# Kernel optimization log

Measured on AMD Instinct MI355X. Metric: run time of the kernel, lower is better.

The kernel has to match this reference:

```python
import jax, jax.numpy as jnp
import numpy as np

EPS_PRE = 1e-05   # constant added to raw scores in the torch module
EPS_NORM = 1e-12  # F.normalize default eps


def setup_inputs() -> dict:
    key = jax.random.key(0)
    kq, kk, kv = jax.random.split(key, 3)
    B, H, S, D = 2, 8, 2048, 64
    query = jax.random.normal(kq, (B, H, S, D), dtype=jnp.float32)
    keys = jax.random.normal(kk, (B, H, S, D), dtype=jnp.float32)
    vals = jax.random.normal(kv, (B, H, S, D), dtype=jnp.float32)
    # causal mask, broadcastable over batch and heads; mask==0 -> score zeroed
    mask = jnp.tril(jnp.ones((S, S), dtype=jnp.int32))[None, None, :, :]
    return {"query": query, "keys": keys, "vals": vals, "mask": mask}


def reference(query, keys, vals, mask):
    # preattn: [B,H,S,S]
    preattn = jnp.einsum("bhsd,bhtd->bhst", query, keys) + EPS_PRE
    preattn = jnp.where(mask == 0, 0.0, preattn)
    # F.normalize(dim=-1): x / max(||x||_2, eps)
    norm = jnp.sqrt(jnp.sum(preattn * preattn, axis=-1, keepdims=True))
    attn = preattn / jnp.maximum(norm, EPS_NORM)
    # dropout is identity in eval mode (reference baseline)
    out = jnp.einsum("bhst,bhtd->bhsd", attn, vals)
    return (out, attn)
```

## Files before the change

### kernel.cpp

```cpp
#include <hip/hip_runtime.h>

#define S_DIM 2048
#define D_DIM 64
#define BH    16
#define EPS_PRE  1e-5f
#define EPS_NORM 1e-12f
#define CT 8

typedef __attribute__((ext_vector_type(8))) short bf8;
typedef __attribute__((ext_vector_type(4))) float f32x4;

static __device__ __forceinline__ unsigned fbits(float x){ union{float f;unsigned u;}v; v.f=x; return v.u; }
static __device__ __forceinline__ float bcast(unsigned u){ union{unsigned u;float f;}v; v.u=u; return v.f; }

static __device__ __forceinline__ void split2(float x, unsigned short& h, unsigned short& l){
  unsigned u = fbits(x);
  h = (unsigned short)(u >> 16);
  float lo = x - bcast(u & 0xffff0000u);
  l = (unsigned short)(fbits(lo) >> 16);
}

static __device__ __forceinline__ void pack4f(float x0, float x1, float x2, float x3,
                                              uint2& hh, uint2& ll){
  unsigned u0=fbits(x0),u1=fbits(x1),u2=fbits(x2),u3=fbits(x3);
  hh.x = (u0>>16) | (u1 & 0xffff0000u);
  hh.y = (u2>>16) | (u3 & 0xffff0000u);
  float l0 = x0 - bcast(u0&0xffff0000u);
  float l1 = x1 - bcast(u1&0xffff0000u);
  float l2 = x2 - bcast(u2&0xffff0000u);
  float l3 = x3 - bcast(u3&0xffff0000u);
  ll.x = (fbits(l0)>>16) | (fbits(l1)&0xffff0000u);
  ll.y = (fbits(l2)>>16) | (fbits(l3)&0xffff0000u);
}

static __device__ __forceinline__ f32x4 mfma16(bf8 a, bf8 b, f32x4 c){
  return __builtin_amdgcn_mfma_f32_16x16x32_bf16(a, b, c, 0, 0, 0);
}

static __device__ __forceinline__ void decode(int c, int& rb, int& ck, int& nk){
  int g = 0;
  while (c >= 4*(g+1)*(g+2)) ++g;
  const int off = c - 4*g*(g+1);
  nk = g + 1;
  const int q = off / nk;
  rb = g*8 + q;
  ck = off - q*nk;
}

__global__ __launch_bounds__(256, 4)
void lka_norm(const float* __restrict__ Qg, const float* __restrict__ Kg,
              float* __restrict__ ssqg, float* __restrict__ Ag)
{
  __shared__ short kThi[4096], kTlo[4096];

  const int tid = threadIdx.x;
  const int wv  = tid >> 6;
  const int ln  = tid & 63;
  const int gq  = ln >> 4;
  const int i16 = ln & 15;

  const int blk = blockIdx.x;
  const int bh  = blk & 15;
  int rb, ck, nk; decode(blk >> 4, rb, ck, nk);
  const int s0 = rb * 64;

  const float* Qb = Qg + (size_t)bh * (S_DIM * D_DIM);
  const float* Kb = Kg + (size_t)bh * (S_DIM * D_DIM);
  float* Ab = Ag + (size_t)bh * ((size_t)S_DIM * S_DIM);

  const int srow = s0 + wv * 16 + i16;

  {
    const int zt0 = (rb + 1) + ((31 - rb) * ck) / nk;
    const int zt1 = (rb + 1) + ((31 - rb) * (ck + 1)) / nk;
    if (zt1 > zt0) {
      const int r = tid >> 2;
      float4* rowp = (float4*)(Ab + (size_t)(s0 + r) * S_DIM + zt0 * 64);
      const int n4 = (zt1 - zt0) * 16;
      float4 z = make_float4(0.f, 0.f, 0.f, 0.f);
      for (int c4 = tid & 3; c4 < n4; c4 += 4) rowp[c4] = z;
    }
  }

  bf8 qhi[2], qlo[2];
  #pragma unroll
  for (int ks = 0; ks < 2; ++ks) {
    const float* qp = Qb + (size_t)srow * D_DIM + ks * 32 + gq * 8;
    float4 a = *(const float4*)qp;
    float4 b = *(const float4*)(qp + 4);
    union { bf8 v; unsigned short h[8]; } H, L;
    float f0[8] = {a.x,a.y,a.z,a.w,b.x,b.y,b.z,b.w};
    #pragma unroll
    for (int j = 0; j < 8; ++j) split2(f0[j], H.h[j], L.h[j]);
    qhi[ks] = H.v; qlo[ks] = L.v;
  }

  auto stageK = [&](int t0){
    const int t  = tid >> 2;
    const int db = (tid & 3) * 16;
    const float* kp = Kb + (size_t)(t0 + t) * D_DIM + db;
    #pragma unroll
    for (int c = 0; c < 4; ++c) {
      float4 kv = *(const float4*)(kp + 4*c);
      uint2 hh, ll; pack4f(kv.x, kv.y, kv.z, kv.w, hh, ll);
      const int idx = t*64 + ((db + 4*c) ^ ((t & 7) << 3));
      *(uint2*)&kThi[idx] = hh;
      *(uint2*)&kTlo[idx] = ll;
    }
  };

  auto qkstep = [&](f32x4* acc){
    #pragma unroll
    for (int rf = 0; rf < 4; ++rf) acc[rf] = (f32x4){0.f,0.f,0.f,0.f};
    #pragma unroll
    for (int ks = 0; ks < 2; ++ks) {
      #pragma unroll
      for (int rf = 0; rf < 4; ++rf) {
        const int t   = rf*16 + i16;
        const int idx = t*64 + ((ks*32 + gq*8) ^ ((t & 7) << 3));
        bf8 ahi = *(const bf8*)&kThi[idx];
        bf8 alo = *(const bf8*)&kTlo[idx];
        acc[rf] = mfma16(ahi, qhi[ks], acc[rf]);
        acc[rf] = mfma16(alo, qhi[ks], acc[rf]);
        acc[rf] = mfma16(ahi, qlo[ks], acc[rf]);
      }
    }
  };

  float ssq = 0.f;
  const int j0 = ck * CT;
  const int j1 = min(j0 + CT, rb + 1);
  for (int j = j0; j < j1; ++j) {
    __syncthreads();
    stageK(j * 64);
    __syncthreads();
    f32x4 acc[4];
    qkstep(acc);
    if (j == rb) {
      #pragma unroll
      for (int rf = 0; rf < 4; ++rf)
        #pragma unroll
        for (int rg = 0; rg < 4; ++rg) {
          const int t = j*64 + rf*16 + gq*4 + rg;
          const float x = (t <= srow) ? (acc[rf][rg] + EPS_PRE) : 0.f;
          ssq += x * x;
        }
    } else {
      #pragma unroll
      for (int rf = 0; rf < 4; ++rf)
        #pragma unroll
        for (int rg = 0; rg < 4; ++rg) {
          const float x = acc[rf][rg] + EPS_PRE;
          ssq += x * x;
        }
    }
  }
  ssq += __shfl_xor(ssq, 16);
  ssq += __shfl_xor(ssq, 32);
  if (gq == 0)
    atomicAdd(&ssqg[bh * S_DIM + srow], ssq);
}

__global__ __launch_bounds__(256, 3)
void lka_emit(const float* __restrict__ Qg, const float* __restrict__ Kg,
              const float* __restrict__ Vg, const float* __restrict__ ssqg,
              float* __restrict__ Og, float* __restrict__ Ag)
{
  __shared__ short kThi[4096], kTlo[4096];
  __shared__ short vThi[4096], vTlo[4096];
  __shared__ short pHi [4096], pLo [4096];

  const int tid = threadIdx.x;
  const int wv  = tid >> 6;
  const int ln  = tid & 63;
  const int gq  = ln >> 4;
  const int i16 = ln & 15;

  const int blk = blockIdx.x;
  const int bh  = blk & 15;
  int rb, ck, nk; decode(blk >> 4, rb, ck, nk);
  (void)nk;
  const int s0 = rb * 64;

  const float* Qb = Qg + (size_t)bh * (S_DIM * D_DIM);
  const float* Kb = Kg + (size_t)bh * (S_DIM * D_DIM);
  const float* Vb = Vg + (size_t)bh * (S_DIM * D_DIM);
  float* Ob = Og + (size_t)bh * (S_DIM * D_DIM);
  float* Ab = Ag + (size_t)bh * ((size_t)S_DIM * S_DIM);

  const int srow = s0 + wv * 16 + i16;

  const float rinv = 1.f / fmaxf(sqrtf(ssqg[bh * S_DIM + srow]), EPS_NORM);

  bf8 qhi[2], qlo[2];
  #pragma unroll
  for (int ks = 0; ks < 2; ++ks) {
    const float* qp = Qb + (size_t)srow * D_DIM + ks * 32 + gq * 8;
    float4 a = *(const float4*)qp;
    float4 b = *(const float4*)(qp + 4);
    union { bf8 v; unsigned short h[8]; } H, L;
    float f0[8] = {a.x,a.y,a.z,a.w,b.x,b.y,b.z,b.w};
    #pragma unroll
    for (int j = 0; j < 8; ++j) split2(f0[j], H.h[j], L.h[j]);
    qhi[ks] = H.v; qlo[ks] = L.v;
  }

  auto stageK = [&](int t0){
    const int t  = tid >> 2;
    const int db = (tid & 3) * 16;
    const float* kp = Kb + (size_t)(t0 + t) * D_DIM + db;
    #pragma unroll
    for (int c = 0; c < 4; ++c) {
      float4 kv = *(const float4*)(kp + 4*c);
      uint2 hh, ll; pack4f(kv.x, kv.y, kv.z, kv.w, hh, ll);
      const int idx = t*64 + ((db + 4*c) ^ ((t & 7) << 3));
      *(uint2*)&kThi[idx] = hh;
      *(uint2*)&kTlo[idx] = ll;
    }
  };
  auto stageV = [&](int t0){
    const int d  = (tid & 31) * 2;
    const int tb = (tid >> 5) * 8;
    float2 rr[8];
    #pragma unroll
    for (int k = 0; k < 8; ++k)
      rr[k] = *(const float2*)(Vb + (size_t)(t0 + tb + k) * D_DIM + d);
    #pragma unroll
    for (int dd = 0; dd < 2; ++dd) {
      union { bf8 v; unsigned short h[8]; } H, L;
      #pragma unroll
      for (int k = 0; k < 8; ++k) split2(dd ? rr[k].y : rr[k].x, H.h[k], L.h[k]);
      const int dc = d + dd;
      const int idx = dc*64 + (tb ^ ((dc & 7) << 3));
      *(bf8*)&vThi[idx] = H.v;
      *(bf8*)&vTlo[idx] = L.v;
    }
  };

  auto qkstep = [&](f32x4* acc){
    #pragma unroll
    for (int rf = 0; rf < 4; ++rf) acc[rf] = (f32x4){0.f,0.f,0.f,0.f};
    #pragma unroll
    for (int ks = 0; ks < 2; ++ks) {
      #pragma unroll
      for (int rf = 0; rf < 4; ++rf) {
        const int t   = rf*16 + i16;
        const int idx = t*64 + ((ks*32 + gq*8) ^ ((t & 7) << 3));
        bf8 ahi = *(const bf8*)&kThi[idx];
        bf8 alo = *(const bf8*)&kTlo[idx];
        acc[rf] = mfma16(ahi, qhi[ks], acc[rf]);
        acc[rf] = mfma16(alo, qhi[ks], acc[rf]);
        acc[rf] = mfma16(ahi, qlo[ks], acc[rf]);
      }
    }
  };

  f32x4 oacc[4];
  #pragma unroll
  for (int rf = 0; rf < 4; ++rf) oacc[rf] = (f32x4){0.f,0.f,0.f,0.f};

  const int pR = wv*16 + i16;

  const int j0 = ck * CT;
  const int j1 = min(j0 + CT, rb + 1);
  for (int j = j0; j < j1; ++j) {
    __syncthreads();
    stageK(j * 64);
    stageV(j * 64);
    __syncthreads();

    f32x4 acc[4];
    qkstep(acc);

    #pragma unroll
    for (int rf = 0; rf < 4; ++rf) {
      f32x4 x;
      #pragma unroll
      for (int rg = 0; rg < 4; ++rg) {
        const int t = j*64 + rf*16 + gq*4 + rg;
        float v = acc[rf][rg] + EPS_PRE;
        if (j == rb && t > srow) v = 0.f;
        x[rg] = v * rinv;
      }
      *(f32x4*)(Ab + (size_t)srow * S_DIM + j*64 + rf*16 + gq*4) = x;
      uint2 hh, ll; pack4f(x[0], x[1], x[2], x[3], hh, ll);
      const int pidx = pR*64 + ((rf*16 + gq*4) ^ ((pR & 7) << 3));
      *(uint2*)&pHi[pidx] = hh;
      *(uint2*)&pLo[pidx] = ll;
    }

    #pragma unroll
    for (int ks = 0; ks < 2; ++ks) {
      const int pi = pR*64 + ((ks*32 + gq*8) ^ ((pR & 7) << 3));
      bf8 bhi = *(const bf8*)&pHi[pi];
      bf8 blo = *(const bf8*)&pLo[pi];
      #pragma unroll
      for (int rfd = 0; rfd < 4; ++rfd) {
        const int dct = rfd*16 + i16;
        const int vi  = dct*64 + ((ks*32 + gq*8) ^ ((dct & 7) << 3));
        bf8 ahi = *(const bf8*)&vThi[vi];
        bf8 alo = *(const bf8*)&vTlo[vi];
        oacc[rfd] = mfma16(ahi, bhi, oacc[rfd]);
        oacc[rfd] = mfma16(alo, bhi, oacc[rfd]);
        oacc[rfd] = mfma16(ahi, blo, oacc[rfd]);
      }
    }
  }

  #pragma unroll
  for (int rfd = 0; rfd < 4; ++rfd)
    #pragma unroll
    for (int rg = 0; rg < 4; ++rg)
      atomicAdd(&Ob[(size_t)srow * D_DIM + rfd*16 + gq*4 + rg], oacc[rfd][rg]);
}

extern "C" void kernel_launch(void* const* d_in, const int* in_sizes, int n_in,
                              void* d_out, int out_size, void* d_ws, size_t ws_size,
                              hipStream_t stream) {
  (void)in_sizes; (void)n_in; (void)out_size; (void)ws_size;
  const float* Q = (const float*)d_in[0];
  const float* K = (const float*)d_in[1];
  const float* V = (const float*)d_in[2];
  float* out  = (float*)d_out;
  float* attn = out + (size_t)BH * S_DIM * D_DIM;
  float* ssq  = (float*)d_ws;

  hipMemsetAsync(ssq, 0, (size_t)BH * S_DIM * sizeof(float), stream);
  hipMemsetAsync(out, 0, (size_t)BH * S_DIM * D_DIM * sizeof(float), stream);

  const int nblk = BH * 80;
  lka_norm<<<dim3(nblk), dim3(256), 0, stream>>>(Q, K, ssq, attn);
  lka_emit<<<dim3(nblk), dim3(256), 0, stream>>>(Q, K, V, ssq, out, attn);
}
```

Baseline: 388.4 us.

## Compute row norms via prefix Gram matrices of K instead of full QK pass

Replaces the row-norm pass, which recomputed every causal QK^T tile, with an algebraic form. Per-tile Gram matrices K^T K and K column sums are built, prefix-summed across tiles, and combined with a single diagonal-tile QK product. Each row's squared norm then comes from q^T M q plus the eps correction terms. This cuts the norm-pass work from quadratic to linear in sequence length and removes the memsets and atomics, at the cost of three extra launches, a larger workspace, and possible cancellation error from the split-bf16 Gram matrix.

```diff
diff --git a/kernel.cpp b/kernel.cpp
--- a/kernel.cpp
+++ b/kernel.cpp
@@ -6,6 +6,12 @@
 #define EPS_PRE  1e-5f
 #define EPS_NORM 1e-12f
 #define CT 8
+
+#define WS_G   0
+#define WS_M   (BH*32*4096)
+#define WS_GV  (2*BH*32*4096)
+#define WS_MV  (WS_GV + BH*32*64)
+#define WS_RI  (WS_MV + BH*32*64)
 
 typedef __attribute__((ext_vector_type(8))) short bf8;
 typedef __attribute__((ext_vector_type(4))) float f32x4;
@@ -37,21 +43,21 @@
   return __builtin_amdgcn_mfma_f32_16x16x32_bf16(a, b, c, 0, 0, 0);
 }
 
-static __device__ __forceinline__ void decode(int c, int& rb, int& ck, int& nk){
+static __device__ __forceinline__ void decode(int c, int& rb, int& ck){
   int g = 0;
   while (c >= 4*(g+1)*(g+2)) ++g;
   const int off = c - 4*g*(g+1);
-  nk = g + 1;
+  const int nk = g + 1;
   const int q = off / nk;
   rb = g*8 + q;
   ck = off - q*nk;
 }
 
 __global__ __launch_bounds__(256, 4)
-void lka_norm(const float* __restrict__ Qg, const float* __restrict__ Kg,
-              float* __restrict__ ssqg, float* __restrict__ Ag)
+void lka_gram(const float* __restrict__ Kg, float* __restrict__ ws,
+              float* __restrict__ Og, float* __restrict__ Ag)
 {
-  __shared__ short kThi[4096], kTlo[4096];
+  __shared__ short tHi[4096], tLo[4096];
 
   const int tid = threadIdx.x;
   const int wv  = tid >> 6;
@@ -61,31 +67,247 @@
 
   const int blk = blockIdx.x;
   const int bh  = blk & 15;
-  int rb, ck, nk; decode(blk >> 4, rb, ck, nk);
-  const int s0 = rb * 64;
+  const int ti  = blk >> 4;
+
+  const float* Kb = Kg + (size_t)bh * (S_DIM * D_DIM);
+
+  {
+    float4 z = make_float4(0.f,0.f,0.f,0.f);
+    float4* p = (float4*)(Og + (size_t)blk * 4096);
+    for (int c = tid; c < 1024; c += 256) p[c] = z;
+  }
+  {
+    const int c0 = (ti + 1) * 64;
+    const int n4 = (S_DIM - c0) >> 2;
+    float* rowp = Ag + (size_t)bh * S_DIM * S_DIM + (size_t)(ti*64 + (tid>>2)) * S_DIM + c0;
+    float4 z = make_float4(0.f,0.f,0.f,0.f);
+    for (int c = tid & 3; c < n4; c += 4) *(float4*)(rowp + 4*c) = z;
+  }
+
+  {
+    const int d  = (tid & 31) * 2;
+    const int tb = (tid >> 5) * 8;
+    float2 rr[8];
+    #pragma unroll
+    for (int k = 0; k < 8; ++k)
+      rr[k] = *(const float2*)(Kb + (size_t)(ti*64 + tb + k) * D_DIM + d);
+    #pragma unroll
+    for (int dd = 0; dd < 2; ++dd) {
+      union { bf8 v; unsigned short h[8]; } H, L;
+      #pragma unroll
+      for (int k = 0; k < 8; ++k) split2(dd ? rr[k].y : rr[k].x, H.h[k], L.h[k]);
+      const int dc = d + dd;
+      const int idx = dc*64 + (tb ^ ((dc & 7) << 3));
+      *(bf8*)&tHi[idx] = H.v;
+      *(bf8*)&tLo[idx] = L.v;
+    }
+  }
+
+  float gsum = 0.f;
+  if (tid < 64) {
+    #pragma unroll 8
+    for (int t = 0; t < 64; ++t) gsum += Kb[(size_t)(ti*64 + t) * D_DIM + tid];
+  }
+  __syncthreads();
+
+  const int d2 = wv*16 + i16;
+  bf8 bhi[2], blo[2];
+  #pragma unroll
+  for (int ks = 0; ks < 2; ++ks) {
+    const int bi = d2*64 + ((ks*32 + gq*8) ^ ((d2 & 7) << 3));
+    bhi[ks] = *(const bf8*)&tHi[bi];
+    blo[ks] = *(const bf8*)&tLo[bi];
+  }
+  f32x4 acc[4];
+  #pragma unroll
+  for (int rf = 0; rf < 4; ++rf) acc[rf] = (f32x4){0.f,0.f,0.f,0.f};
+  #pragma unroll
+  for (int ks = 0; ks < 2; ++ks) {
+    #pragma unroll
+    for (int rf = 0; rf < 4; ++rf) {
+      const int d1 = rf*16 + i16;
+      const int ai = d1*64 + ((ks*32 + gq*8) ^ ((d1 & 7) << 3));
+      bf8 ahi = *(const bf8*)&tHi[ai];
+      bf8 alo = *(const bf8*)&tLo[ai];
+      acc[rf] = mfma16(ahi, bhi[ks], acc[rf]);
+      acc[rf] = mfma16(alo, bhi[ks], acc[rf]);
+      acc[rf] = mfma16(ahi, blo[ks], acc[rf]);
+    }
+  }
+  float* Gp = ws + WS_G + (size_t)(bh*32 + ti) * 4096;
+  #pragma unroll
+  for (int rf = 0; rf < 4; ++rf)
+    *(f32x4*)(Gp + d2*64 + rf*16 + gq*4) = acc[rf];
+
+  if (tid < 64) ws[WS_GV + (size_t)(bh*32 + ti)*64 + tid] = gsum;
+}
+
+__global__ __launch_bounds__(256, 8)
+void lka_prefix(float* __restrict__ ws)
+{
+  const int tid = threadIdx.x;
+  const int blk = blockIdx.x;
+  const int bh  = blk >> 2;
+  const int r4  = blk & 3;
+
+  const int row = r4*16 + (tid >> 4);
+  const int c4  = (tid & 15) * 4;
+
+  const float* Gp = ws + WS_G + (size_t)(bh*32)*4096 + row*64 + c4;
+  float*       Mp = ws + WS_M + (size_t)(bh*32)*4096 + row*64 + c4;
+
+  f32x4 acc = (f32x4){0.f,0.f,0.f,0.f};
+  #pragma unroll 4
+  for (int i = 0; i < 32; ++i) {
+    *(f32x4*)(Mp + (size_t)i*4096) = acc;
+    f32x4 g = *(const f32x4*)(Gp + (size_t)i*4096);
+    acc[0]+=g[0]; acc[1]+=g[1]; acc[2]+=g[2]; acc[3]+=g[3];
+  }
+
+  if (r4 == 0 && tid < 64) {
+    float a = 0.f;
+    #pragma unroll 4
+    for (int i = 0; i < 32; ++i) {
+      ws[WS_MV + (size_t)(bh*32 + i)*64 + tid] = a;
+      a += ws[WS_GV + (size_t)(bh*32 + i)*64 + tid];
+    }
+  }
+}
+
+__global__ __launch_bounds__(256, 4)
+void lka_rownorm(const float* __restrict__ Qg, const float* __restrict__ Kg,
+                 float* __restrict__ ws)
+{
+  __shared__ short kHi[4096], kLo[4096];
+  __shared__ short mHi[4096], mLo[4096];
+  __shared__ float mvS[64];
+
+  const int tid = threadIdx.x;
+  const int wv  = tid >> 6;
+  const int ln  = tid & 63;
+  const int gq  = ln >> 4;
+  const int i16 = ln & 15;
+
+  const int blk = blockIdx.x;
+  const int bh  = blk & 15;
+  const int rb  = blk >> 4;
+  const int s0  = rb * 64;
 
   const float* Qb = Qg + (size_t)bh * (S_DIM * D_DIM);
   const float* Kb = Kg + (size_t)bh * (S_DIM * D_DIM);
+
+  const int srow = s0 + wv*16 + i16;
+
+  {
+    const int r  = tid >> 2;
+    const int db = (tid & 3) * 16;
+    const float* kp = Kb + (size_t)(s0 + r) * D_DIM + db;
+    const float* mp = ws + WS_M + (size_t)(bh*32 + rb)*4096 + r*64 + db;
+    #pragma unroll
+    for (int c = 0; c < 4; ++c) {
+      float4 kv = *(const float4*)(kp + 4*c);
+      uint2 hh, ll; pack4f(kv.x, kv.y, kv.z, kv.w, hh, ll);
+      const int idx = r*64 + ((db + 4*c) ^ ((r & 7) << 3));
+      *(uint2*)&kHi[idx] = hh;
+      *(uint2*)&kLo[idx] = ll;
+      float4 mv = *(const float4*)(mp + 4*c);
+      uint2 mh, mlo; pack4f(mv.x, mv.y, mv.z, mv.w, mh, mlo);
+      *(uint2*)&mHi[idx] = mh;
+      *(uint2*)&mLo[idx] = mlo;
+    }
+  }
+  if (tid < 64) mvS[tid] = ws[WS_MV + (size_t)(bh*32 + rb)*64 + tid];
+
+  bf8 qhi[2], qlo[2];
+  #pragma unroll
+  for (int ks = 0; ks < 2; ++ks) {
+    const float* qp = Qb + (size_t)srow * D_DIM + ks*32 + gq*8;
+    float4 a = *(const float4*)qp;
+    float4 b = *(const float4*)(qp + 4);
+    union { bf8 v; unsigned short h[8]; } H, L;
+    float f0[8] = {a.x,a.y,a.z,a.w,b.x,b.y,b.z,b.w};
+    #pragma unroll
+    for (int j = 0; j < 8; ++j) split2(f0[j], H.h[j], L.h[j]);
+    qhi[ks] = H.v; qlo[ks] = L.v;
+  }
+  __syncthreads();
+
+  f32x4 accS[4], accY[4];
+  #pragma unroll
+  for (int rf = 0; rf < 4; ++rf) { accS[rf] = (f32x4){0.f,0.f,0.f,0.f}; accY[rf] = (f32x4){0.f,0.f,0.f,0.f}; }
+  #pragma unroll
+  for (int ks = 0; ks < 2; ++ks) {
+    #pragma unroll
+    for (int rf = 0; rf < 4; ++rf) {
+      const int r   = rf*16 + i16;
+      const int idx = r*64 + ((ks*32 + gq*8) ^ ((r & 7) << 3));
+      bf8 ahi = *(const bf8*)&kHi[idx];
+      bf8 alo = *(const bf8*)&kLo[idx];
+      accS[rf] = mfma16(ahi, qhi[ks], accS[rf]);
+      accS[rf] = mfma16(alo, qhi[ks], accS[rf]);
+      accS[rf] = mfma16(ahi, qlo[ks], accS[rf]);
+      bf8 Ahi = *(const bf8*)&mHi[idx];
+      bf8 Alo = *(const bf8*)&mLo[idx];
+      accY[rf] = mfma16(Ahi, qhi[ks], accY[rf]);
+      accY[rf] = mfma16(Alo, qhi[ks], accY[rf]);
+      accY[rf] = mfma16(Ahi, qlo[ks], accY[rf]);
+    }
+  }
+
+  float ssq = 0.f;
+  #pragma unroll
+  for (int rf = 0; rf < 4; ++rf) {
+    f32x4 q4 = *(const f32x4*)(Qb + (size_t)srow * D_DIM + rf*16 + gq*4);
+    f32x4 m4 = *(const f32x4*)&mvS[rf*16 + gq*4];
+    #pragma unroll
+    for (int rg = 0; rg < 4; ++rg) {
+      ssq += q4[rg] * (accY[rf][rg] + 2.f*EPS_PRE*m4[rg]);
+      const int t = s0 + rf*16 + gq*4 + rg;
+      if (t <= srow) { const float x = accS[rf][rg] + EPS_PRE; ssq += x*x; }
+    }
+  }
+  ssq += __shfl_xor(ssq, 16);
+  ssq += __shfl_xor(ssq, 32);
+  ssq += EPS_PRE*EPS_PRE * (float)(rb*64);
+  ssq = fmaxf(ssq, 0.f);
+  const float rinv = 1.f / fmaxf(sqrtf(ssq), EPS_NORM);
+  if (gq == 0) ws[WS_RI + (size_t)bh*S_DIM + srow] = rinv;
+}
+
+__global__ __launch_bounds__(256, 3)
+void lka_emit(const float* __restrict__ Qg, const float* __restrict__ Kg,
+              const float* __restrict__ Vg, const float* __restrict__ ws,
+              float* __restrict__ Og, float* __restrict__ Ag)
+{
+  __shared__ short kThi[4096], kTlo[4096];
+  __shared__ short vThi[4096], vTlo[4096];
+  __shared__ short pHi [4096], pLo [4096];
+
+  const int tid = threadIdx.x;
+  const int wv  = tid >> 6;
+  const int ln  = tid & 63;
+  const int gq  = ln >> 4;
+  const int i16 = ln & 15;
+
+  const int blk = blockIdx.x;
+  const int bh  = blk & 15;
+  int rb, ck; decode(blk >> 4, rb, ck);
+  const int s0 = rb * 64;
+
+  const float* Qb = Qg + (size_t)bh * (S_DIM * D_DIM);
+  const float* Kb = Kg + (size_t)bh * (S_DIM * D_DIM);
+  const float* Vb = Vg + (size_t)bh * (S_DIM * D_DIM);
+  float* Ob = Og + (size_t)bh * (S_DIM * D_DIM);
   float* Ab = Ag + (size_t)bh * ((size_t)S_DIM * S_DIM);
 
-  const int srow = s0 + wv * 16 + i16;
-
-  {
-    const int zt0 = (rb + 1) + ((31 - rb) * ck) / nk;
-    const int zt1 = (rb + 1) + ((31 - rb) * (ck + 1)) / nk;
-    if (zt1 > zt0) {
-      const int r = tid >> 2;
-      float4* rowp = (float4*)(Ab + (size_t)(s0 + r) * S_DIM + zt0 * 64);
-      const int n4 = (zt1 - zt0) * 16;
-      float4 z = make_float4(0.f, 0.f, 0.f, 0.f);
-      for (int c4 = tid & 3; c4 < n4; c4 += 4) rowp[c4] = z;
-    }
-  }
+  const int srow = s0 + wv*16 + i16;
+
+  const float rinv = ws[WS_RI + (size_t)bh*S_DIM + srow];
 
   bf8 qhi[2], qlo[2];
   #pragma unroll
   for (int ks = 0; ks < 2; ++ks) {
-    const float* qp = Qb + (size_t)srow * D_DIM + ks * 32 + gq * 8;
+    const float* qp = Qb + (size_t)srow * D_DIM + ks*32 + gq*8;
     float4 a = *(const float4*)qp;
     float4 b = *(const float4*)(qp + 4);
     union { bf8 v; unsigned short h[8]; } H, L;
@@ -108,8 +330,40 @@
       *(uint2*)&kTlo[idx] = ll;
     }
   };
-
-  auto qkstep = [&](f32x4* acc){
+  auto stageV = [&](int t0){
+    const int d  = (tid & 31) * 2;
+    const int tb = (tid >> 5) * 8;
+    float2 rr[8];
+    #pragma unroll
+    for (int k = 0; k < 8; ++k)
+      rr[k] = *(const float2*)(Vb + (size_t)(t0 + tb + k) * D_DIM + d);
+    #pragma unroll
+    for (int dd = 0; dd < 2; ++dd) {
+      union { bf8 v; unsigned short h[8]; } H, L;
+      #pragma unroll
+      for (int k = 0; k < 8; ++k) split2(dd ? rr[k].y : rr[k].x, H.h[k], L.h[k]);
+      const int dc = d + dd;
+      const int idx = dc*64 + (tb ^ ((dc & 7) << 3));
+      *(bf8*)&vThi[idx] = H.v;
+      *(bf8*)&vTlo[idx] = L.v;
+    }
+  };
+
+  f32x4 oacc[4];
+  #pragma unroll
+  for (int rf = 0; rf < 4; ++rf) oacc[rf] = (f32x4){0.f,0.f,0.f,0.f};
+
+  const int pR = wv*16 + i16;
+
+  const int j0 = ck * CT;
+  const int j1 = min(j0 + CT, rb + 1);
+  for (int j = j0; j < j1; ++j) {
+    __syncthreads();
+    stageK(j * 64);
+    stageV(j * 64);
+    __syncthreads();
+
+    f32x4 acc[4];
     #pragma unroll
     for (int rf = 0; rf < 4; ++rf) acc[rf] = (f32x4){0.f,0.f,0.f,0.f};
     #pragma unroll
@@ -125,152 +379,6 @@
         acc[rf] = mfma16(ahi, qlo[ks], acc[rf]);
       }
     }
-  };
-
-  float ssq = 0.f;
-  const int j0 = ck * CT;
-  const int j1 = min(j0 + CT, rb + 1);
-  for (int j = j0; j < j1; ++j) {
-    __syncthreads();
-    stageK(j * 64);
-    __syncthreads();
-    f32x4 acc[4];
-    qkstep(acc);
-    if (j == rb) {
-      #pragma unroll
-      for (int rf = 0; rf < 4; ++rf)
-        #pragma unroll
-        for (int rg = 0; rg < 4; ++rg) {
-          const int t = j*64 + rf*16 + gq*4 + rg;
-          const float x = (t <= srow) ? (acc[rf][rg] + EPS_PRE) : 0.f;
-          ssq += x * x;
-        }
-    } else {
-      #pragma unroll
-      for (int rf = 0; rf < 4; ++rf)
-        #pragma unroll
-        for (int rg = 0; rg < 4; ++rg) {
-          const float x = acc[rf][rg] + EPS_PRE;
-          ssq += x * x;
-        }
-    }
-  }
-  ssq += __shfl_xor(ssq, 16);
-  ssq += __shfl_xor(ssq, 32);
-  if (gq == 0)
-    atomicAdd(&ssqg[bh * S_DIM + srow], ssq);
-}
-
-__global__ __launch_bounds__(256, 3)
-void lka_emit(const float* __restrict__ Qg, const float* __restrict__ Kg,
-              const float* __restrict__ Vg, const float* __restrict__ ssqg,
-              float* __restrict__ Og, float* __restrict__ Ag)
-{
-  __shared__ short kThi[4096], kTlo[4096];
-  __shared__ short vThi[4096], vTlo[4096];
-  __shared__ short pHi [4096], pLo [4096];
-
-  const int tid = threadIdx.x;
-  const int wv  = tid >> 6;
-  const int ln  = tid & 63;
-  const int gq  = ln >> 4;
-  const int i16 = ln & 15;
-
-  const int blk = blockIdx.x;
-  const int bh  = blk & 15;
-  int rb, ck, nk; decode(blk >> 4, rb, ck, nk);
-  (void)nk;
-  const int s0 = rb * 64;
-
-  const float* Qb = Qg + (size_t)bh * (S_DIM * D_DIM);
-  const float* Kb = Kg + (size_t)bh * (S_DIM * D_DIM);
-  const float* Vb = Vg + (size_t)bh * (S_DIM * D_DIM);
-  float* Ob = Og + (size_t)bh * (S_DIM * D_DIM);
-  float* Ab = Ag + (size_t)bh * ((size_t)S_DIM * S_DIM);
-
-  const int srow = s0 + wv * 16 + i16;
-
-  const float rinv = 1.f / fmaxf(sqrtf(ssqg[bh * S_DIM + srow]), EPS_NORM);
-
-  bf8 qhi[2], qlo[2];
-  #pragma unroll
-  for (int ks = 0; ks < 2; ++ks) {
-    const float* qp = Qb + (size_t)srow * D_DIM + ks * 32 + gq * 8;
-    float4 a = *(const float4*)qp;
-    float4 b = *(const float4*)(qp + 4);
-    union { bf8 v; unsigned short h[8]; } H, L;
-    float f0[8] = {a.x,a.y,a.z,a.w,b.x,b.y,b.z,b.w};
-    #pragma unroll
-    for (int j = 0; j < 8; ++j) split2(f0[j], H.h[j], L.h[j]);
-    qhi[ks] = H.v; qlo[ks] = L.v;
-  }
-
-  auto stageK = [&](int t0){
-    const int t  = tid >> 2;
-    const int db = (tid & 3) * 16;
-    const float* kp = Kb + (size_t)(t0 + t) * D_DIM + db;
-    #pragma unroll
-    for (int c = 0; c < 4; ++c) {
-      float4 kv = *(const float4*)(kp + 4*c);
-      uint2 hh, ll; pack4f(kv.x, kv.y, kv.z, kv.w, hh, ll);
-      const int idx = t*64 + ((db + 4*c) ^ ((t & 7) << 3));
-      *(uint2*)&kThi[idx] = hh;
-      *(uint2*)&kTlo[idx] = ll;
-    }
-  };
-  auto stageV = [&](int t0){
-    const int d  = (tid & 31) * 2;
-    const int tb = (tid >> 5) * 8;
-    float2 rr[8];
-    #pragma unroll
-    for (int k = 0; k < 8; ++k)
-      rr[k] = *(const float2*)(Vb + (size_t)(t0 + tb + k) * D_DIM + d);
-    #pragma unroll
-    for (int dd = 0; dd < 2; ++dd) {
-      union { bf8 v; unsigned short h[8]; } H, L;
-      #pragma unroll
-      for (int k = 0; k < 8; ++k) split2(dd ? rr[k].y : rr[k].x, H.h[k], L.h[k]);
-      const int dc = d + dd;
-      const int idx = dc*64 + (tb ^ ((dc & 7) << 3));
-      *(bf8*)&vThi[idx] = H.v;
-      *(bf8*)&vTlo[idx] = L.v;
-    }
-  };
-
-  auto qkstep = [&](f32x4* acc){
-    #pragma unroll
-    for (int rf = 0; rf < 4; ++rf) acc[rf] = (f32x4){0.f,0.f,0.f,0.f};
-    #pragma unroll
-    for (int ks = 0; ks < 2; ++ks) {
-      #pragma unroll
-      for (int rf = 0; rf < 4; ++rf) {
-        const int t   = rf*16 + i16;
-        const int idx = t*64 + ((ks*32 + gq*8) ^ ((t & 7) << 3));
-        bf8 ahi = *(const bf8*)&kThi[idx];
-        bf8 alo = *(const bf8*)&kTlo[idx];
-        acc[rf] = mfma16(ahi, qhi[ks], acc[rf]);
-        acc[rf] = mfma16(alo, qhi[ks], acc[rf]);
-        acc[rf] = mfma16(ahi, qlo[ks], acc[rf]);
-      }
-    }
-  };
-
-  f32x4 oacc[4];
-  #pragma unroll
-  for (int rf = 0; rf < 4; ++rf) oacc[rf] = (f32x4){0.f,0.f,0.f,0.f};
-
-  const int pR = wv*16 + i16;
-
-  const int j0 = ck * CT;
-  const int j1 = min(j0 + CT, rb + 1);
-  for (int j = j0; j < j1; ++j) {
-    __syncthreads();
-    stageK(j * 64);
-    stageV(j * 64);
-    __syncthreads();
-
-    f32x4 acc[4];
-    qkstep(acc);
 
     #pragma unroll
     for (int rf = 0; rf < 4; ++rf) {
@@ -323,12 +431,10 @@
   const float* V = (const float*)d_in[2];
   float* out  = (float*)d_out;
   float* attn = out + (size_t)BH * S_DIM * D_DIM;
-  float* ssq  = (float*)d_ws;
-
-  hipMemsetAsync(ssq, 0, (size_t)BH * S_DIM * sizeof(float), stream);
-  hipMemsetAsync(out, 0, (size_t)BH * S_DIM * D_DIM * sizeof(float), stream);
-
-  const int nblk = BH * 80;
-  lka_norm<<<dim3(nblk), dim3(256), 0, stream>>>(Q, K, ssq, attn);
-  lka_emit<<<dim3(nblk), dim3(256), 0, stream>>>(Q, K, V, ssq, out, attn);
-}
+  float* ws   = (float*)d_ws;
+
+  lka_gram   <<<dim3(512),  dim3(256), 0, stream>>>(K, ws, out, attn);
+  lka_prefix <<<dim3(64),   dim3(256), 0, stream>>>(ws);
+  lka_rownorm<<<dim3(512),  dim3(256), 0, stream>>>(Q, K, ws);
+  lka_emit   <<<dim3(BH*80),dim3(256), 0, stream>>>(Q, K, V, ws, out, attn);
+}
```

After: 445.8 us. +14.8%, slower.
